# Optimization experiments

Hardware: AMD Instinct MI355X
Metric: run time of the kernel (lower is better)

The kernel has to match this reference:

```python
import jax, jax.numpy as jnp
import numpy as np

N_NODES = 50000
N_EDGES = 800000
IN_DIM = 128
HID = 32
HEADS = 4
OUT_DIM = 2
NEG_SLOPE = 0.2


def gat_conv(feat, W, al, ar, bias, src, dst, n_nodes):
    """DGL GATConv (eval mode, no dropout). feat: [N, Fin]; W: [Fin, H*D];
    al, ar: [H, D]; bias: [H*D]. Returns [N, H, D]."""
    H, D = al.shape
    hf = (feat @ W).reshape(n_nodes, H, D)              # [N,H,D]
    el = jnp.einsum('nhd,hd->nh', hf, al)               # [N,H]
    er = jnp.einsum('nhd,hd->nh', hf, ar)               # [N,H]
    e = el[src] + er[dst]                               # [E,H]
    e = jax.nn.leaky_relu(e, NEG_SLOPE)
    # segment softmax over incoming edges of each dst node
    emax = jax.ops.segment_max(e, dst, num_segments=n_nodes)  # [N,H]
    emax = jnp.where(jnp.isfinite(emax), emax, 0.0)
    ex = jnp.exp(e - emax[dst])                         # [E,H]
    denom = jax.ops.segment_sum(ex, dst, num_segments=n_nodes)  # [N,H]
    alpha = ex / jnp.maximum(denom[dst], 1e-30)         # [E,H]
    msg = hf[src] * alpha[:, :, None]                   # [E,H,D]
    out = jax.ops.segment_sum(msg, dst, num_segments=n_nodes)   # [N,H,D]
    return out + bias.reshape(1, H, D)


def setup_inputs() -> dict:
    key = jax.random.key(0)
    ks = jax.random.split(key, 16)
    f32 = jnp.float32
    in_feat = jax.random.normal(ks[0], (N_NODES, IN_DIM), dtype=f32)
    src = jax.random.randint(ks[1], (N_EDGES,), 0, N_NODES)
    dst = jax.random.randint(ks[2], (N_EDGES,), 0, N_NODES)
    s1 = 1.0 / np.sqrt(IN_DIM)
    s2 = 1.0 / np.sqrt(HID * HEADS)
    W1 = jax.random.normal(ks[3], (IN_DIM, HEADS * HID), dtype=f32) * s1
    al1 = jax.random.normal(ks[4], (HEADS, HID), dtype=f32) * 0.1
    ar1 = jax.random.normal(ks[5], (HEADS, HID), dtype=f32) * 0.1
    b1 = jnp.zeros((HEADS * HID,), dtype=f32)
    W2 = jax.random.normal(ks[6], (HEADS * HID, HEADS * HID), dtype=f32) * s2
    al2 = jax.random.normal(ks[7], (HEADS, HID), dtype=f32) * 0.1
    ar2 = jax.random.normal(ks[8], (HEADS, HID), dtype=f32) * 0.1
    b2 = jnp.zeros((HEADS * HID,), dtype=f32)
    Wout = jax.random.normal(ks[9], (HID, OUT_DIM), dtype=f32) * (1.0 / np.sqrt(HID))
    bout = jnp.zeros((OUT_DIM,), dtype=f32)
    return {"in_feat": in_feat, "W1": W1, "al1": al1, "ar1": ar1, "b1": b1,
            "W2": W2, "al2": al2, "ar2": ar2, "b2": b2,
            "Wout": Wout, "bout": bout, "src": src, "dst": dst}


def reference(in_feat, W1, al1, ar1, b1, W2, al2, ar2, b2, Wout, bout, src, dst):
    h = gat_conv(in_feat, W1, al1, ar1, b1, src, dst, N_NODES)  # [N,H,D]
    h = jax.nn.relu(h.reshape(N_NODES, HEADS * HID))            # flatten(1) + relu
    h = gat_conv(h, W2, al2, ar2, b2, src, dst, N_NODES)        # [N,H,D]
    emd = h.mean(axis=1)                                        # mean over heads -> [N,D]
    logits = jax.nn.relu(emd) @ Wout + bout                     # [N,2]
    return jax.nn.softmax(logits, axis=-1)
```

## Files before the change

kernel.cpp:

```cpp
#include <hip/hip_runtime.h>
#include <cmath>

#define N_NODES 50000
#define N_EDGES 800000
#define NBUCK 196
#define NHB 196
#define EPB 4096

typedef unsigned short u16;
typedef unsigned int u32;
typedef __attribute__((ext_vector_type(8))) short bf16x8;
typedef __attribute__((ext_vector_type(4))) float f32x4;

static __device__ __forceinline__ float lrelu(float x) { return x > 0.f ? x : 0.2f * x; }
static __device__ __forceinline__ float bf2f(u16 u) { return __uint_as_float(((u32)u) << 16); }
static __device__ __forceinline__ u16 f2bf(float f) {
    u32 b = __float_as_uint(f);
    return (u16)((b + 0x7FFFu + ((b >> 16) & 1u)) >> 16);
}
static __device__ __forceinline__ u32 pack2(float a, float b) {
    return (u32)f2bf(a) | ((u32)f2bf(b) << 16);
}
static __device__ __forceinline__ float sx(u32 u, int k) {
    return (float)((int)(u << ((3 - k) * 8)) >> 24);
}

__global__ __launch_bounds__(1024) void bhist_pack_k(const int* __restrict__ dst, u32* __restrict__ bcnt,
                                                     const float* __restrict__ W1, const float* __restrict__ W2,
                                                     u16* __restrict__ Wp1, u16* __restrict__ Wp2,
                                                     u32* __restrict__ done) {
    int tid = threadIdx.x;
    if (blockIdx.x < NHB) {
        __shared__ u32 hist[NBUCK];
        for (int i = tid; i < NBUCK; i += 1024) hist[i] = 0;
        __syncthreads();
        int base = blockIdx.x * EPB;
#pragma unroll
        for (int k = 0; k < 4; ++k) {
            int e = base + k * 1024 + tid;
            if (e < N_EDGES) atomicAdd(&hist[dst[e] >> 8], 1u);
        }
        __syncthreads();
        for (int i = tid; i < NBUCK; i += 1024) bcnt[(size_t)i * NHB + blockIdx.x] = hist[i];
    } else {
        if (blockIdx.x == NHB && tid == 0) *done = 0;
        int gi = (blockIdx.x - NHB) * 1024 + tid;
        const float* W = (gi < 16384) ? W1 : W2;
        u16* Wp = (gi < 16384) ? Wp1 : Wp2;
        int i = gi & 16383;
        int j = i & 7, lane = (i >> 3) & 63, ks = (i >> 9) & 3, nt = i >> 11;
        int k = ks * 32 + (lane >> 4) * 8 + j;
        int ncol = nt * 16 + (lane & 15);
        Wp[i] = f2bf(W[k * 128 + ncol]);
    }
}

__global__ __launch_bounds__(256) void scant_k(const u32* __restrict__ bcnt, u32* __restrict__ wbase,
                                               u32* __restrict__ btot, int* __restrict__ bstart,
                                               u32* __restrict__ done) {
    __shared__ u32 s[256];
    __shared__ bool amLast;
    int i = blockIdx.x, t = threadIdx.x;
    u32 v = (t < NHB) ? bcnt[(size_t)i * NHB + t] : 0;
    s[t] = v;
    __syncthreads();
    for (int o = 1; o < 256; o <<= 1) {
        u32 x = (t >= o) ? s[t - o] : 0;
        __syncthreads();
        s[t] += x;
        __syncthreads();
    }
    if (t < NHB) wbase[(size_t)i * NHB + t] = s[t] - v;
    if (t == 255) atomicExch(&btot[i], s[255]);
    __threadfence();
    if (t == 0) amLast = (atomicAdd(done, 1u) == NBUCK - 1);
    __syncthreads();
    if (!amLast) return;
    __threadfence();
    u32 v2 = (t < NBUCK) ? atomicAdd(&btot[t], 0u) : 0;
    s[t] = v2;
    __syncthreads();
    for (int o = 1; o < 256; o <<= 1) {
        u32 x = (t >= o) ? s[t - o] : 0;
        __syncthreads();
        s[t] += x;
        __syncthreads();
    }
    if (t < NBUCK) bstart[t] = (int)(s[t] - v2);
    if (t == NBUCK - 1) bstart[NBUCK] = (int)s[t];
}

__global__ __launch_bounds__(1024) void bscatter_k(const int* __restrict__ src, const int* __restrict__ dst,
                                                   const u32* __restrict__ wbase, const int* __restrict__ bstart,
                                                   u32* __restrict__ bucketed) {
    __shared__ u32 pos[NBUCK];
    int tid = threadIdx.x;
    for (int i = tid; i < NBUCK; i += 1024)
        pos[i] = (u32)bstart[i] + wbase[(size_t)i * NHB + blockIdx.x];
    __syncthreads();
    int base = blockIdx.x * EPB;
#pragma unroll
    for (int k = 0; k < 4; ++k) {
        int e = base + k * 1024 + tid;
        if (e < N_EDGES) {
            int d = dst[e];
            int b = d >> 8;
            u32 p = atomicAdd(&pos[b], 1u);
            bucketed[p] = (u32)src[e] | ((u32)(d & 255) << 16);
        }
    }
}

__global__ __launch_bounds__(1024) void bcsr_gemm1_k(
    const u32* __restrict__ bucketed, const int* __restrict__ bstart,
    int* __restrict__ offs, u16* __restrict__ srcs,
    const float* __restrict__ X, const u16* __restrict__ Wp,
    const float* __restrict__ al, const float* __restrict__ ar,
    signed char* __restrict__ hq, float2* __restrict__ elhs, float* __restrict__ er, int n)
{
    __shared__ u16 xs[256][136];
    int tid = threadIdx.x;

    if (blockIdx.x < NBUCK) {
        u32* cnt = (u32*)&xs[0][0];
        int* s   = (int*)(cnt + 256);
        u32* fp  = (u32*)(s + 256);
        int b = blockIdx.x;
        int ebeg = bstart[b], eend = bstart[b + 1];
        int ne = eend - ebeg;
        if (tid < 256) cnt[tid] = 0;
        __syncthreads();
        for (int i = tid; i < ne; i += 1024)
            atomicAdd(&cnt[bucketed[ebeg + i] >> 16], 1u);
        __syncthreads();
        if (tid < 256) s[tid] = (int)cnt[tid];
        __syncthreads();
        for (int o = 1; o < 256; o <<= 1) {
            int v = (tid < 256 && tid >= o) ? s[tid - o] : 0;
            __syncthreads();
            if (tid < 256) s[tid] += v;
            __syncthreads();
        }
        if (tid < 256) {
            int excl = s[tid] - (int)cnt[tid];
            int node = b * 256 + tid;
            if (node < N_NODES) offs[node] = ebeg + excl;
            fp[tid] = (u32)excl;
        }
        if (b == NBUCK - 1 && tid == 0) offs[N_NODES] = N_EDGES;
        __syncthreads();
        for (int i = tid; i < ne; i += 1024) {
            u32 u = bucketed[ebeg + i];
            u32 p = atomicAdd(&fp[u >> 16], 1u);
            srcs[ebeg + p] = (u16)(u & 0xFFFFu);
        }
        return;
    }

    int row0 = (blockIdx.x - NBUCK) * 256;
    const float4* X4 = (const float4*)X;
    for (int i = tid; i < 8192; i += 1024) {
        int r = i >> 5, c = i & 31;
        float4 v = make_float4(0.f, 0.f, 0.f, 0.f);
        if (row0 + r < n) v = X4[(size_t)(row0 + r) * 32 + c];
        ((uint2*)&xs[r][0])[c] = make_uint2(pack2(v.x, v.y), pack2(v.z, v.w));
    }
    __syncthreads();

    int wave = tid >> 6, lane = tid & 63;
    int hd = wave & 3, wrow = (wave >> 2) * 64;
    int quad = lane >> 4, l15 = lane & 15;

    bf16x8 bfrag[2][4];
#pragma unroll
    for (int ct = 0; ct < 2; ++ct) {
        int nt = hd * 2 + ct;
#pragma unroll
        for (int ks = 0; ks < 4; ++ks)
            bfrag[ct][ks] = *(const bf16x8*)(Wp + ((((nt * 4 + ks) * 64) + lane) << 3));
    }

    f32x4 acc[4][2];
#pragma unroll
    for (int rt = 0; rt < 4; ++rt)
#pragma unroll
        for (int ct = 0; ct < 2; ++ct)
            acc[rt][ct] = (f32x4){0.f, 0.f, 0.f, 0.f};

#pragma unroll
    for (int ks = 0; ks < 4; ++ks) {
#pragma unroll
        for (int rt = 0; rt < 4; ++rt) {
            bf16x8 a = *(const bf16x8*)&xs[wrow + rt * 16 + l15][ks * 32 + quad * 8];
            acc[rt][0] = __builtin_amdgcn_mfma_f32_16x16x32_bf16(a, bfrag[0][ks], acc[rt][0], 0, 0, 0);
            acc[rt][1] = __builtin_amdgcn_mfma_f32_16x16x32_bf16(a, bfrag[1][ks], acc[rt][1], 0, 0, 0);
        }
    }

    float alv0 = al[hd * 32 + l15], alv1 = al[hd * 32 + 16 + l15];
    float arv0 = ar[hd * 32 + l15], arv1 = ar[hd * 32 + 16 + l15];
#pragma unroll
    for (int rt = 0; rt < 4; ++rt) {
#pragma unroll
        for (int r = 0; r < 4; ++r) {
            int row = row0 + wrow + rt * 16 + quad * 4 + r;
            float c0 = acc[rt][0][r], c1 = acc[rt][1][r];
            float m = fmaxf(fabsf(c0), fabsf(c1));
            m = fmaxf(m, __shfl_xor(m, 1));
            m = fmaxf(m, __shfl_xor(m, 2));
            m = fmaxf(m, __shfl_xor(m, 4));
            m = fmaxf(m, __shfl_xor(m, 8));
            m = fmaxf(m, 1e-20f);
            float qsc = 127.0f / m;
            if (row < n) {
                hq[(size_t)row * 128 + hd * 32 + l15] = (signed char)(int)rintf(c0 * qsc);
                hq[(size_t)row * 128 + hd * 32 + 16 + l15] = (signed char)(int)rintf(c1 * qsc);
            }
            float pel = c0 * alv0 + c1 * alv1;
            float per = c0 * arv0 + c1 * arv1;
            pel += __shfl_xor(pel, 1); pel += __shfl_xor(pel, 2);
            pel += __shfl_xor(pel, 4); pel += __shfl_xor(pel, 8);
            per += __shfl_xor(per, 1); per += __shfl_xor(per, 2);
            per += __shfl_xor(per, 4); per += __shfl_xor(per, 8);
            if (l15 == 0 && row < n) {
                elhs[row * 4 + hd] = make_float2(pel, m * (1.0f / 127.0f));
                er[row * 4 + hd] = per;
            }
        }
    }
}

template <int BF16IN>
__global__ __launch_bounds__(256) void gemm_mfma(
    const void* __restrict__ Xv, const u16* __restrict__ Wp,
    const float* __restrict__ al, const float* __restrict__ ar,
    signed char* __restrict__ hq, float2* __restrict__ elhs, float* __restrict__ er, int n)
{
    __shared__ u16 xs[64][136];
    int row0 = blockIdx.x * 64;
    int tid = threadIdx.x;
    if (BF16IN) {
        const uint4* Xb = (const uint4*)Xv;
        for (int i = tid; i < 1024; i += 256) {
            int r = i >> 4, c = i & 15;
            uint4 v = make_uint4(0u, 0u, 0u, 0u);
            if (row0 + r < n) v = Xb[(size_t)(row0 + r) * 16 + c];
            ((uint4*)&xs[r][0])[c] = v;
        }
    } else {
        const float4* X4 = (const float4*)Xv;
        for (int i = tid; i < 2048; i += 256) {
            int r = i >> 5, c = i & 31;
            float4 v = make_float4(0.f, 0.f, 0.f, 0.f);
            if (row0 + r < n) v = X4[(size_t)(row0 + r) * 32 + c];
            ((uint2*)&xs[r][0])[c] = make_uint2(pack2(v.x, v.y), pack2(v.z, v.w));
        }
    }
    __syncthreads();

    int wave = tid >> 6, lane = tid & 63;
    int quad = lane >> 4, l15 = lane & 15;

    bf16x8 bfrag[2][4];
#pragma unroll
    for (int ct = 0; ct < 2; ++ct) {
        int nt = wave * 2 + ct;
#pragma unroll
        for (int ks = 0; ks < 4; ++ks)
            bfrag[ct][ks] = *(const bf16x8*)(Wp + ((((nt * 4 + ks) * 64) + lane) << 3));
    }

    f32x4 acc[4][2];
#pragma unroll
    for (int rt = 0; rt < 4; ++rt)
#pragma unroll
        for (int ct = 0; ct < 2; ++ct)
            acc[rt][ct] = (f32x4){0.f, 0.f, 0.f, 0.f};

#pragma unroll
    for (int ks = 0; ks < 4; ++ks) {
#pragma unroll
        for (int rt = 0; rt < 4; ++rt) {
            bf16x8 a = *(const bf16x8*)&xs[rt * 16 + l15][ks * 32 + quad * 8];
            acc[rt][0] = __builtin_amdgcn_mfma_f32_16x16x32_bf16(a, bfrag[0][ks], acc[rt][0], 0, 0, 0);
            acc[rt][1] = __builtin_amdgcn_mfma_f32_16x16x32_bf16(a, bfrag[1][ks], acc[rt][1], 0, 0, 0);
        }
    }

    float alv0 = al[wave * 32 + l15], alv1 = al[wave * 32 + 16 + l15];
    float arv0 = ar[wave * 32 + l15], arv1 = ar[wave * 32 + 16 + l15];
#pragma unroll
    for (int rt = 0; rt < 4; ++rt) {
#pragma unroll
        for (int r = 0; r < 4; ++r) {
            int row = row0 + rt * 16 + quad * 4 + r;
            float c0 = acc[rt][0][r], c1 = acc[rt][1][r];
            float m = fmaxf(fabsf(c0), fabsf(c1));
            m = fmaxf(m, __shfl_xor(m, 1));
            m = fmaxf(m, __shfl_xor(m, 2));
            m = fmaxf(m, __shfl_xor(m, 4));
            m = fmaxf(m, __shfl_xor(m, 8));
            m = fmaxf(m, 1e-20f);
            float qsc = 127.0f / m;
            if (row < n) {
                hq[(size_t)row * 128 + wave * 32 + l15] = (signed char)(int)rintf(c0 * qsc);
                hq[(size_t)row * 128 + wave * 32 + 16 + l15] = (signed char)(int)rintf(c1 * qsc);
            }
            float pel = c0 * alv0 + c1 * alv1;
            float per = c0 * arv0 + c1 * arv1;
            pel += __shfl_xor(pel, 1); pel += __shfl_xor(pel, 2);
            pel += __shfl_xor(pel, 4); pel += __shfl_xor(pel, 8);
            per += __shfl_xor(per, 1); per += __shfl_xor(per, 2);
            per += __shfl_xor(per, 4); per += __shfl_xor(per, 8);
            if (l15 == 0 && row < n) {
                elhs[row * 4 + wave] = make_float2(pel, m * (1.0f / 127.0f));
                er[row * 4 + wave] = per;
            }
        }
    }
}

static __device__ __forceinline__ void agg_core(
    int node, int lane, const int* __restrict__ offs, const u16* __restrict__ srcs,
    const float2* __restrict__ elhs, const float* __restrict__ er,
    const signed char* __restrict__ hq,
    float acc[8], float& den)
{
    int qw = lane >> 4;
    int q = lane & 15;
    int h = q >> 2;
    float erh = er[node * 4 + h];
    int beg = offs[node], end = offs[node + 1];
    int deg = end - beg;
    den = 0.f;
#pragma unroll
    for (int i = 0; i < 8; i++) acc[i] = 0.f;

    if (deg <= 64) {
        int psrc = (lane < deg) ? (int)srcs[beg + lane] : 0;
        int base = beg;
        for (; base + 16 <= end; base += 16) {
            int j = base - beg + qw;
            int ss[4];
            ss[0] = __shfl(psrc, j);
            ss[1] = __shfl(psrc, j + 4);
            ss[2] = __shfl(psrc, j + 8);
            ss[3] = __shfl(psrc, j + 12);
            float2 eh[4];
            uint2 uv[4];
#pragma unroll
            for (int k = 0; k < 4; ++k) {
                eh[k] = elhs[ss[k] * 4 + h];
                uv[k] = *(const uint2*)(hq + (size_t)ss[k] * 128 + q * 8);
            }
#pragma unroll
            for (int k = 0; k < 4; ++k) {
                float w = __expf(lrelu(eh[k].x + erh));
                float ws = w * eh[k].y;
                den += w;
                acc[0] += ws * sx(uv[k].x, 0);
                acc[1] += ws * sx(uv[k].x, 1);
                acc[2] += ws * sx(uv[k].x, 2);
                acc[3] += ws * sx(uv[k].x, 3);
                acc[4] += ws * sx(uv[k].y, 0);
                acc[5] += ws * sx(uv[k].y, 1);
                acc[6] += ws * sx(uv[k].y, 2);
                acc[7] += ws * sx(uv[k].y, 3);
            }
        }
        for (; base + 8 <= end; base += 8) {
            int j = base - beg + qw;
            int s0 = __shfl(psrc, j);
            int s1 = __shfl(psrc, j + 4);
            float2 e0 = elhs[s0 * 4 + h], e1 = elhs[s1 * 4 + h];
            uint2 u0 = *(const uint2*)(hq + (size_t)s0 * 128 + q * 8);
            uint2 u1 = *(const uint2*)(hq + (size_t)s1 * 128 + q * 8);
            float w0 = __expf(lrelu(e0.x + erh));
            float w1 = __expf(lrelu(e1.x + erh));
            float ws0 = w0 * e0.y, ws1 = w1 * e1.y;
            den += w0 + w1;
            acc[0] += ws0 * sx(u0.x, 0) + ws1 * sx(u1.x, 0);
            acc[1] += ws0 * sx(u0.x, 1) + ws1 * sx(u1.x, 1);
            acc[2] += ws0 * sx(u0.x, 2) + ws1 * sx(u1.x, 2);
            acc[3] += ws0 * sx(u0.x, 3) + ws1 * sx(u1.x, 3);
            acc[4] += ws0 * sx(u0.y, 0) + ws1 * sx(u1.y, 0);
            acc[5] += ws0 * sx(u0.y, 1) + ws1 * sx(u1.y, 1);
            acc[6] += ws0 * sx(u0.y, 2) + ws1 * sx(u1.y, 2);
            acc[7] += ws0 * sx(u0.y, 3) + ws1 * sx(u1.y, 3);
        }
        for (; base < end; base += 4) {
            int e = base + qw;
            bool valid = e < end;
            int j = valid ? (e - beg) : 0;
            int s = __shfl(psrc, j);
            float2 eh = elhs[s * 4 + h];
            float w = valid ? __expf(lrelu(eh.x + erh)) : 0.f;
            float ws = w * eh.y;
            uint2 u = *(const uint2*)(hq + (size_t)s * 128 + q * 8);
            den += w;
            acc[0] += ws * sx(u.x, 0);
            acc[1] += ws * sx(u.x, 1);
            acc[2] += ws * sx(u.x, 2);
            acc[3] += ws * sx(u.x, 3);
            acc[4] += ws * sx(u.y, 0);
            acc[5] += ws * sx(u.y, 1);
            acc[6] += ws * sx(u.y, 2);
            acc[7] += ws * sx(u.y, 3);
        }
    } else {
        for (int base = beg; base < end; base += 4) {
            int e = base + qw;
            bool valid = e < end;
            int ec = valid ? e : end - 1;
            int s = srcs[ec];
            float2 eh = elhs[s * 4 + h];
            float w = valid ? __expf(lrelu(eh.x + erh)) : 0.f;
            float ws = w * eh.y;
            uint2 u = *(const uint2*)(hq + (size_t)s * 128 + q * 8);
            den += w;
            acc[0] += ws * sx(u.x, 0);
            acc[1] += ws * sx(u.x, 1);
            acc[2] += ws * sx(u.x, 2);
            acc[3] += ws * sx(u.x, 3);
            acc[4] += ws * sx(u.y, 0);
            acc[5] += ws * sx(u.y, 1);
            acc[6] += ws * sx(u.y, 2);
            acc[7] += ws * sx(u.y, 3);
        }
    }
#pragma unroll
    for (int i = 0; i < 8; i++) {
        acc[i] += __shfl_xor(acc[i], 16);
        acc[i] += __shfl_xor(acc[i], 32);
    }
    den += __shfl_xor(den, 16);
    den += __shfl_xor(den, 32);
}

__global__ __launch_bounds__(256) void agg1_k(const int* __restrict__ offs, const u16* __restrict__ srcs,
                                              const float2* __restrict__ elhs, const float* __restrict__ er,
                                              const signed char* __restrict__ hq,
                                              const float* __restrict__ bias, u16* __restrict__ h1) {
    int node = blockIdx.x * 4 + (threadIdx.x >> 6);
    int lane = threadIdx.x & 63;
    if (node >= N_NODES) return;
    float acc[8], den;
    agg_core(node, lane, offs, srcs, elhs, er, hq, acc, den);
    int qw = lane >> 4, q = lane & 15;
    if (qw == 0) {
        float inv = 1.0f / fmaxf(den, 1e-30f);
        float o[8];
#pragma unroll
        for (int i = 0; i < 8; i++)
            o[i] = fmaxf(acc[i] * inv + bias[q * 8 + i], 0.f);
        uint4 pk;
        pk.x = pack2(o[0], o[1]);
        pk.y = pack2(o[2], o[3]);
        pk.z = pack2(o[4], o[5]);
        pk.w = pack2(o[6], o[7]);
        *(uint4*)(h1 + (size_t)node * 128 + q * 8) = pk;
    }
}

__global__ __launch_bounds__(256) void agg2_k(const int* __restrict__ offs, const u16* __restrict__ srcs,
                                              const float2* __restrict__ elhs, const float* __restrict__ er,
                                              const signed char* __restrict__ hq,
                                              const float* __restrict__ bias,
                                              const float* __restrict__ Wout, const float* __restrict__ bout,
                                              float2* __restrict__ out) {
    int node = blockIdx.x * 4 + (threadIdx.x >> 6);
    int lane = threadIdx.x & 63;
    if (node >= N_NODES) return;
    float acc[8], den;
    agg_core(node, lane, offs, srcs, elhs, er, hq, acc, den);
    int q = lane & 15;
    float inv = 1.0f / fmaxf(den, 1e-30f);
    float o[8];
#pragma unroll
    for (int i = 0; i < 8; i++) o[i] = acc[i] * inv + bias[q * 8 + i];
#pragma unroll
    for (int i = 0; i < 8; i++) {
        o[i] += __shfl_xor(o[i], 4);
        o[i] += __shfl_xor(o[i], 8);
        o[i] = fmaxf(0.25f * o[i], 0.f);
    }
    int d0 = (q & 3) * 8;
    float l0 = 0.f, l1 = 0.f;
#pragma unroll
    for (int i = 0; i < 8; i++) {
        l0 += o[i] * Wout[(d0 + i) * 2];
        l1 += o[i] * Wout[(d0 + i) * 2 + 1];
    }
    l0 += __shfl_xor(l0, 1); l0 += __shfl_xor(l0, 2);
    l1 += __shfl_xor(l1, 1); l1 += __shfl_xor(l1, 2);
    if (lane == 0) {
        l0 += bout[0];
        l1 += bout[1];
        float mx = fmaxf(l0, l1);
        float e0 = __expf(l0 - mx), e1 = __expf(l1 - mx);
        float invs = 1.f / (e0 + e1);
        out[node] = make_float2(e0 * invs, e1 * invs);
    }
}

extern "C" void kernel_launch(void* const* d_in, const int* in_sizes, int n_in,
                              void* d_out, int out_size, void* d_ws, size_t ws_size,
                              hipStream_t stream) {
    const float* in_feat = (const float*)d_in[0];
    const float* W1   = (const float*)d_in[1];
    const float* al1  = (const float*)d_in[2];
    const float* ar1  = (const float*)d_in[3];
    const float* b1   = (const float*)d_in[4];
    const float* W2   = (const float*)d_in[5];
    const float* al2  = (const float*)d_in[6];
    const float* ar2  = (const float*)d_in[7];
    const float* b2   = (const float*)d_in[8];
    const float* Wout = (const float*)d_in[9];
    const float* bout = (const float*)d_in[10];
    const int*   src  = (const int*)d_in[11];
    const int*   dst  = (const int*)d_in[12];
    float* out = (float*)d_out;

    char* ws = (char*)d_ws;
    size_t off = 0;
    auto carve = [&](size_t bytes) {
        char* p = ws + off;
        off = (off + bytes + 255) & ~(size_t)255;
        return p;
    };
    signed char* hq  = (signed char*)carve((size_t)N_NODES * 128);
    float2* elhs     = (float2*)carve((size_t)N_NODES * 4 * 8);
    float* er        = (float*)carve((size_t)N_NODES * 4 * 4);
    u16*   h1        = (u16*)carve((size_t)N_NODES * 128 * 2);
    u16*   srcs      = (u16*)carve((size_t)N_EDGES * 2);
    u32*   bucketed  = (u32*)carve((size_t)N_EDGES * 4);
    u32*   bcnt      = (u32*)carve((size_t)NBUCK * NHB * 4);
    u32*   wbase     = (u32*)carve((size_t)NBUCK * NHB * 4);
    u32*   btot      = (u32*)carve((size_t)NBUCK * 4);
    int*   bstart    = (int*)carve((size_t)(NBUCK + 1) * 4);
    int*   offs      = (int*)carve((size_t)(N_NODES + 1) * 4);
    u16*   Wp1       = (u16*)carve((size_t)16384 * 2);
    u16*   Wp2       = (u16*)carve((size_t)16384 * 2);
    u32*   done      = (u32*)carve(256);
    (void)ws_size; (void)in_sizes; (void)n_in; (void)out_size;

    const int GB   = (N_NODES + 63) / 64;
    const int GB256 = (N_NODES + 255) / 256;
    const int AB   = (N_NODES + 3) / 4;

    bhist_pack_k<<<NHB + 32, 1024, 0, stream>>>(dst, bcnt, W1, W2, Wp1, Wp2, done);
    scant_k<<<NBUCK, 256, 0, stream>>>(bcnt, wbase, btot, bstart, done);
    bscatter_k<<<NHB, 1024, 0, stream>>>(src, dst, wbase, bstart, bucketed);
    bcsr_gemm1_k<<<NBUCK + GB256, 1024, 0, stream>>>(bucketed, bstart, offs, srcs,
                                                     in_feat, Wp1, al1, ar1, hq, elhs, er, N_NODES);
    agg1_k<<<AB, 256, 0, stream>>>(offs, srcs, elhs, er, hq, b1, h1);
    gemm_mfma<1><<<GB, 256, 0, stream>>>(h1, Wp2, al2, ar2, hq, elhs, er, N_NODES);
    agg2_k<<<AB, 256, 0, stream>>>(offs, srcs, elhs, er, hq, b2, Wout, bout, (float2*)out);
}
```

Baseline: 220.6 us.

## Split bucket scan into separate kernel and shrink fused CSR/GEMM1 blocks to 256 threads

Replaces the last-block-done atomic pattern in the bucket scan with a separate single-block kernel that scans the bucket totals, which removes the done counter and the threadfence/atomic traffic. The fused CSR-build plus first-layer GEMM kernel goes from 1024-thread blocks over 256 rows to 256-thread blocks over 64 rows, with less shared memory per block. The CSR part now runs 256 threads per bucket, so each thread handles more edges. This looks like a partial revert to an earlier configuration, and it adds one more kernel launch.

```diff
diff --git a/kernel.cpp b/kernel.cpp
--- a/kernel.cpp
+++ b/kernel.cpp
@@ -13,7 +13,6 @@
 typedef __attribute__((ext_vector_type(4))) float f32x4;
 
 static __device__ __forceinline__ float lrelu(float x) { return x > 0.f ? x : 0.2f * x; }
-static __device__ __forceinline__ float bf2f(u16 u) { return __uint_as_float(((u32)u) << 16); }
 static __device__ __forceinline__ u16 f2bf(float f) {
     u32 b = __float_as_uint(f);
     return (u16)((b + 0x7FFFu + ((b >> 16) & 1u)) >> 16);
@@ -27,8 +26,7 @@
 
 __global__ __launch_bounds__(1024) void bhist_pack_k(const int* __restrict__ dst, u32* __restrict__ bcnt,
                                                      const float* __restrict__ W1, const float* __restrict__ W2,
-                                                     u16* __restrict__ Wp1, u16* __restrict__ Wp2,
-                                                     u32* __restrict__ done) {
+                                                     u16* __restrict__ Wp1, u16* __restrict__ Wp2) {
     int tid = threadIdx.x;
     if (blockIdx.x < NHB) {
         __shared__ u32 hist[NBUCK];
@@ -43,7 +41,6 @@
         __syncthreads();
         for (int i = tid; i < NBUCK; i += 1024) bcnt[(size_t)i * NHB + blockIdx.x] = hist[i];
     } else {
-        if (blockIdx.x == NHB && tid == 0) *done = 0;
         int gi = (blockIdx.x - NHB) * 1024 + tid;
         const float* W = (gi < 16384) ? W1 : W2;
         u16* Wp = (gi < 16384) ? Wp1 : Wp2;
@@ -56,10 +53,8 @@
 }
 
 __global__ __launch_bounds__(256) void scant_k(const u32* __restrict__ bcnt, u32* __restrict__ wbase,
-                                               u32* __restrict__ btot, int* __restrict__ bstart,
-                                               u32* __restrict__ done) {
+                                               u32* __restrict__ btot) {
     __shared__ u32 s[256];
-    __shared__ bool amLast;
     int i = blockIdx.x, t = threadIdx.x;
     u32 v = (t < NHB) ? bcnt[(size_t)i * NHB + t] : 0;
     s[t] = v;
@@ -71,14 +66,14 @@
         __syncthreads();
     }
     if (t < NHB) wbase[(size_t)i * NHB + t] = s[t] - v;
-    if (t == 255) atomicExch(&btot[i], s[255]);
-    __threadfence();
-    if (t == 0) amLast = (atomicAdd(done, 1u) == NBUCK - 1);
-    __syncthreads();
-    if (!amLast) return;
-    __threadfence();
-    u32 v2 = (t < NBUCK) ? atomicAdd(&btot[t], 0u) : 0;
-    s[t] = v2;
+    if (t == 255) btot[i] = s[255];
+}
+
+__global__ __launch_bounds__(256) void scanb2_k(const u32* __restrict__ btot, int* __restrict__ bstart) {
+    __shared__ u32 s[256];
+    int t = threadIdx.x;
+    u32 v = (t < NBUCK) ? btot[t] : 0;
+    s[t] = v;
     __syncthreads();
     for (int o = 1; o < 256; o <<= 1) {
         u32 x = (t >= o) ? s[t - o] : 0;
@@ -86,7 +81,7 @@
         s[t] += x;
         __syncthreads();
     }
-    if (t < NBUCK) bstart[t] = (int)(s[t] - v2);
+    if (t < NBUCK) bstart[t] = (int)(s[t] - v);
     if (t == NBUCK - 1) bstart[NBUCK] = (int)s[t];
 }
 
@@ -111,14 +106,14 @@
     }
 }
 
-__global__ __launch_bounds__(1024) void bcsr_gemm1_k(
+__global__ __launch_bounds__(256) void bcsr_gemm1_k(
     const u32* __restrict__ bucketed, const int* __restrict__ bstart,
     int* __restrict__ offs, u16* __restrict__ srcs,
     const float* __restrict__ X, const u16* __restrict__ Wp,
     const float* __restrict__ al, const float* __restrict__ ar,
     signed char* __restrict__ hq, float2* __restrict__ elhs, float* __restrict__ er, int n)
 {
-    __shared__ u16 xs[256][136];
+    __shared__ u16 xs[64][136];
     int tid = threadIdx.x;
 
     if (blockIdx.x < NBUCK) {
@@ -128,28 +123,26 @@
         int b = blockIdx.x;
         int ebeg = bstart[b], eend = bstart[b + 1];
         int ne = eend - ebeg;
-        if (tid < 256) cnt[tid] = 0;
-        __syncthreads();
-        for (int i = tid; i < ne; i += 1024)
+        cnt[tid] = 0;
+        __syncthreads();
+        for (int i = tid; i < ne; i += 256)
             atomicAdd(&cnt[bucketed[ebeg + i] >> 16], 1u);
         __syncthreads();
-        if (tid < 256) s[tid] = (int)cnt[tid];
+        s[tid] = (int)cnt[tid];
         __syncthreads();
         for (int o = 1; o < 256; o <<= 1) {
-            int v = (tid < 256 && tid >= o) ? s[tid - o] : 0;
+            int v = (tid >= o) ? s[tid - o] : 0;
             __syncthreads();
-            if (tid < 256) s[tid] += v;
+            s[tid] += v;
             __syncthreads();
         }
-        if (tid < 256) {
-            int excl = s[tid] - (int)cnt[tid];
-            int node = b * 256 + tid;
-            if (node < N_NODES) offs[node] = ebeg + excl;
-            fp[tid] = (u32)excl;
-        }
+        int excl = s[tid] - (int)cnt[tid];
+        int node = b * 256 + tid;
+        if (node < N_NODES) offs[node] = ebeg + excl;
         if (b == NBUCK - 1 && tid == 0) offs[N_NODES] = N_EDGES;
-        __syncthreads();
-        for (int i = tid; i < ne; i += 1024) {
+        fp[tid] = (u32)excl;
+        __syncthreads();
+        for (int i = tid; i < ne; i += 256) {
             u32 u = bucketed[ebeg + i];
             u32 p = atomicAdd(&fp[u >> 16], 1u);
             srcs[ebeg + p] = (u16)(u & 0xFFFFu);
@@ -157,104 +150,13 @@
         return;
     }
 
-    int row0 = (blockIdx.x - NBUCK) * 256;
+    int row0 = (blockIdx.x - NBUCK) * 64;
     const float4* X4 = (const float4*)X;
-    for (int i = tid; i < 8192; i += 1024) {
+    for (int i = tid; i < 2048; i += 256) {
         int r = i >> 5, c = i & 31;
         float4 v = make_float4(0.f, 0.f, 0.f, 0.f);
         if (row0 + r < n) v = X4[(size_t)(row0 + r) * 32 + c];
         ((uint2*)&xs[r][0])[c] = make_uint2(pack2(v.x, v.y), pack2(v.z, v.w));
-    }
-    __syncthreads();
-
-    int wave = tid >> 6, lane = tid & 63;
-    int hd = wave & 3, wrow = (wave >> 2) * 64;
-    int quad = lane >> 4, l15 = lane & 15;
-
-    bf16x8 bfrag[2][4];
-#pragma unroll
-    for (int ct = 0; ct < 2; ++ct) {
-        int nt = hd * 2 + ct;
-#pragma unroll
-        for (int ks = 0; ks < 4; ++ks)
-            bfrag[ct][ks] = *(const bf16x8*)(Wp + ((((nt * 4 + ks) * 64) + lane) << 3));
-    }
-
-    f32x4 acc[4][2];
-#pragma unroll
-    for (int rt = 0; rt < 4; ++rt)
-#pragma unroll
-        for (int ct = 0; ct < 2; ++ct)
-            acc[rt][ct] = (f32x4){0.f, 0.f, 0.f, 0.f};
-
-#pragma unroll
-    for (int ks = 0; ks < 4; ++ks) {
-#pragma unroll
-        for (int rt = 0; rt < 4; ++rt) {
-            bf16x8 a = *(const bf16x8*)&xs[wrow + rt * 16 + l15][ks * 32 + quad * 8];
-            acc[rt][0] = __builtin_amdgcn_mfma_f32_16x16x32_bf16(a, bfrag[0][ks], acc[rt][0], 0, 0, 0);
-            acc[rt][1] = __builtin_amdgcn_mfma_f32_16x16x32_bf16(a, bfrag[1][ks], acc[rt][1], 0, 0, 0);
-        }
-    }
-
-    float alv0 = al[hd * 32 + l15], alv1 = al[hd * 32 + 16 + l15];
-    float arv0 = ar[hd * 32 + l15], arv1 = ar[hd * 32 + 16 + l15];
-#pragma unroll
-    for (int rt = 0; rt < 4; ++rt) {
-#pragma unroll
-        for (int r = 0; r < 4; ++r) {
-            int row = row0 + wrow + rt * 16 + quad * 4 + r;
-            float c0 = acc[rt][0][r], c1 = acc[rt][1][r];
-            float m = fmaxf(fabsf(c0), fabsf(c1));
-            m = fmaxf(m, __shfl_xor(m, 1));
-            m = fmaxf(m, __shfl_xor(m, 2));
-            m = fmaxf(m, __shfl_xor(m, 4));
-            m = fmaxf(m, __shfl_xor(m, 8));
-            m = fmaxf(m, 1e-20f);
-            float qsc = 127.0f / m;
-            if (row < n) {
-                hq[(size_t)row * 128 + hd * 32 + l15] = (signed char)(int)rintf(c0 * qsc);
-                hq[(size_t)row * 128 + hd * 32 + 16 + l15] = (signed char)(int)rintf(c1 * qsc);
-            }
-            float pel = c0 * alv0 + c1 * alv1;
-            float per = c0 * arv0 + c1 * arv1;
-            pel += __shfl_xor(pel, 1); pel += __shfl_xor(pel, 2);
-            pel += __shfl_xor(pel, 4); pel += __shfl_xor(pel, 8);
-            per += __shfl_xor(per, 1); per += __shfl_xor(per, 2);
-            per += __shfl_xor(per, 4); per += __shfl_xor(per, 8);
-            if (l15 == 0 && row < n) {
-                elhs[row * 4 + hd] = make_float2(pel, m * (1.0f / 127.0f));
-                er[row * 4 + hd] = per;
-            }
-        }
-    }
-}
-
-template <int BF16IN>
-__global__ __launch_bounds__(256) void gemm_mfma(
-    const void* __restrict__ Xv, const u16* __restrict__ Wp,
-    const float* __restrict__ al, const float* __restrict__ ar,
-    signed char* __restrict__ hq, float2* __restrict__ elhs, float* __restrict__ er, int n)
-{
-    __shared__ u16 xs[64][136];
-    int row0 = blockIdx.x * 64;
-    int tid = threadIdx.x;
-    if (BF16IN) {
-        const uint4* Xb = (const uint4*)Xv;
-        for (int i = tid; i < 1024; i += 256) {
-            int r = i >> 4, c = i & 15;
-            uint4 v = make_uint4(0u, 0u, 0u, 0u);
-            if (row0 + r < n) v = Xb[(size_t)(row0 + r) * 16 + c];
-            ((uint4*)&xs[r][0])[c] = v;
-        }
-    } else {
-        const float4* X4 = (const float4*)Xv;
-        for (int i = tid; i < 2048; i += 256) {
-            int r = i >> 5, c = i & 31;
-            float4 v = make_float4(0.f, 0.f, 0.f, 0.f);
-            if (row0 + r < n) v = X4[(size_t)(row0 + r) * 32 + c];
-            ((uint2*)&xs[r][0])[c] = make_uint2(pack2(v.x, v.y), pack2(v.z, v.w));
-        }
     }
     __syncthreads();
 
@@ -320,6 +222,96 @@
     }
 }
 
+template <int BF16IN>
+__global__ __launch_bounds__(256) void gemm_mfma(
+    const void* __restrict__ Xv, const u16* __restrict__ Wp,
+    const float* __restrict__ al, const float* __restrict__ ar,
+    signed char* __restrict__ hq, float2* __restrict__ elhs, float* __restrict__ er, int n)
+{
+    __shared__ u16 xs[64][136];
+    int row0 = blockIdx.x * 64;
+    int tid = threadIdx.x;
+    if (BF16IN) {
+        const uint4* Xb = (const uint4*)Xv;
+        for (int i = tid; i < 1024; i += 256) {
+            int r = i >> 4, c = i & 15;
+            uint4 v = make_uint4(0u, 0u, 0u, 0u);
+            if (row0 + r < n) v = Xb[(size_t)(row0 + r) * 16 + c];
+            ((uint4*)&xs[r][0])[c] = v;
+        }
+    } else {
+        const float4* X4 = (const float4*)Xv;
+        for (int i = tid; i < 2048; i += 256) {
+            int r = i >> 5, c = i & 31;
+            float4 v = make_float4(0.f, 0.f, 0.f, 0.f);
+            if (row0 + r < n) v = X4[(size_t)(row0 + r) * 32 + c];
+            ((uint2*)&xs[r][0])[c] = make_uint2(pack2(v.x, v.y), pack2(v.z, v.w));
+        }
+    }
+    __syncthreads();
+
+    int wave = tid >> 6, lane = tid & 63;
+    int quad = lane >> 4, l15 = lane & 15;
+
+    bf16x8 bfrag[2][4];
+#pragma unroll
+    for (int ct = 0; ct < 2; ++ct) {
+        int nt = wave * 2 + ct;
+#pragma unroll
+        for (int ks = 0; ks < 4; ++ks)
+            bfrag[ct][ks] = *(const bf16x8*)(Wp + ((((nt * 4 + ks) * 64) + lane) << 3));
+    }
+
+    f32x4 acc[4][2];
+#pragma unroll
+    for (int rt = 0; rt < 4; ++rt)
+#pragma unroll
+        for (int ct = 0; ct < 2; ++ct)
+            acc[rt][ct] = (f32x4){0.f, 0.f, 0.f, 0.f};
+
+#pragma unroll
+    for (int ks = 0; ks < 4; ++ks) {
+#pragma unroll
+        for (int rt = 0; rt < 4; ++rt) {
+            bf16x8 a = *(const bf16x8*)&xs[rt * 16 + l15][ks * 32 + quad * 8];
+            acc[rt][0] = __builtin_amdgcn_mfma_f32_16x16x32_bf16(a, bfrag[0][ks], acc[rt][0], 0, 0, 0);
+            acc[rt][1] = __builtin_amdgcn_mfma_f32_16x16x32_bf16(a, bfrag[1][ks], acc[rt][1], 0, 0, 0);
+        }
+    }
+
+    float alv0 = al[wave * 32 + l15], alv1 = al[wave * 32 + 16 + l15];
+    float arv0 = ar[wave * 32 + l15], arv1 = ar[wave * 32 + 16 + l15];
+#pragma unroll
+    for (int rt = 0; rt < 4; ++rt) {
+#pragma unroll
+        for (int r = 0; r < 4; ++r) {
+            int row = row0 + rt * 16 + quad * 4 + r;
+            float c0 = acc[rt][0][r], c1 = acc[rt][1][r];
+            float m = fmaxf(fabsf(c0), fabsf(c1));
+            m = fmaxf(m, __shfl_xor(m, 1));
+            m = fmaxf(m, __shfl_xor(m, 2));
+            m = fmaxf(m, __shfl_xor(m, 4));
+            m = fmaxf(m, __shfl_xor(m, 8));
+            m = fmaxf(m, 1e-20f);
+            float qsc = 127.0f / m;
+            if (row < n) {
+                hq[(size_t)row * 128 + wave * 32 + l15] = (signed char)(int)rintf(c0 * qsc);
+                hq[(size_t)row * 128 + wave * 32 + 16 + l15] = (signed char)(int)rintf(c1 * qsc);
+            }
+            float pel = c0 * alv0 + c1 * alv1;
+            float per = c0 * arv0 + c1 * arv1;
+            pel += __shfl_xor(pel, 1); pel += __shfl_xor(pel, 2);
+            pel += __shfl_xor(pel, 4); pel += __shfl_xor(pel, 8);
+            per += __shfl_xor(per, 1); per += __shfl_xor(per, 2);
+            per += __shfl_xor(per, 4); per += __shfl_xor(per, 8);
+            if (l15 == 0 && row < n) {
+                elhs[row * 4 + wave] = make_float2(pel, m * (1.0f / 127.0f));
+                er[row * 4 + wave] = per;
+            }
+        }
+    }
+}
+
 static __device__ __forceinline__ void agg_core(
     int node, int lane, const int* __restrict__ offs, const u16* __restrict__ srcs,
     const float2* __restrict__ elhs, const float* __restrict__ er,
@@ -530,8 +522,8 @@
     };
     signed char* hq  = (signed char*)carve((size_t)N_NODES * 128);
     float2* elhs     = (float2*)carve((size_t)N_NODES * 4 * 8);
+    u16*   h1        = (u16*)carve((size_t)N_NODES * 128 * 2);
     float* er        = (float*)carve((size_t)N_NODES * 4 * 4);
-    u16*   h1        = (u16*)carve((size_t)N_NODES * 128 * 2);
     u16*   srcs      = (u16*)carve((size_t)N_EDGES * 2);
     u32*   bucketed  = (u32*)carve((size_t)N_EDGES * 4);
     u32*   bcnt      = (u32*)carve((size_t)NBUCK * NHB * 4);
@@ -541,19 +533,21 @@
     int*   offs      = (int*)carve((size_t)(N_NODES + 1) * 4);
     u16*   Wp1       = (u16*)carve((size_t)16384 * 2);
     u16*   Wp2       = (u16*)carve((size_t)16384 * 2);
-    u32*   done      = (u32*)carve(256);
     (void)ws_size; (void)in_sizes; (void)n_in; (void)out_size;
 
-    const int GB   = (N_NODES + 63) / 64;
-    const int GB256 = (N_NODES + 255) / 256;
-    const int AB   = (N_NODES + 3) / 4;
-
-    bhist_pack_k<<<NHB + 32, 1024, 0, stream>>>(dst, bcnt, W1, W2, Wp1, Wp2, done);
-    scant_k<<<NBUCK, 256, 0, stream>>>(bcnt, wbase, btot, bstart, done);
+    const int GB = (N_NODES + 63) / 64;
+    const int AB = (N_NODES + 3) / 4;
+
+    bhist_pack_k<<<NHB + 32, 1024, 0, stream>>>(dst, bcnt, W1, W2, Wp1, Wp2);
+    scant_k<<<NBUCK, 256, 0, stream>>>(bcnt, wbase, btot);
+    scanb2_k<<<1, 256, 0, stream>>>(btot, bstart);
     bscatter_k<<<NHB, 1024, 0, stream>>>(src, dst, wbase, bstart, bucketed);
-    bcsr_gemm1_k<<<NBUCK + GB256, 1024, 0, stream>>>(bucketed, bstart, offs, srcs,
-                                                     in_feat, Wp1, al1, ar1, hq, elhs, er, N_NODES);
+
+    bcsr_gemm1_k<<<NBUCK + GB, 256, 0, stream>>>(bucketed, bstart, offs, srcs,
+                                                 in_feat, Wp1, al1, ar1, hq, elhs, er, N_NODES);
+
     agg1_k<<<AB, 256, 0, stream>>>(offs, srcs, elhs, er, hq, b1, h1);
+
     gemm_mfma<1><<<GB, 256, 0, stream>>>(h1, Wp2, al2, ar2, hq, elhs, er, N_NODES);
     agg2_k<<<AB, 256, 0, stream>>>(offs, srcs, elhs, er, hq, b2, Wout, bout, (float2*)out);
 }
```

New measurement: 203.4 us. 7.8% less time.
